# Kernel optimization log

Measured on AMD Instinct MI355X. Metric: run time of the kernel, lower is better.

## Reference

```python
import jax, jax.numpy as jnp
import numpy as np

E, D, F, K = 8, 1024, 2048, 2  # n_experts, d_model, d_ff, top_k


def setup_inputs() -> dict:
    key = jax.random.key(0)
    ks = jax.random.split(key, 6)
    s = 0.02
    return {
        "x": jax.random.normal(ks[0], (4, 2048, D), dtype=jnp.float32),
        "Wr": jax.random.normal(ks[1], (E, D), dtype=jnp.float32) * s,  # router Linear weight (no bias)
        "W1": jax.random.normal(ks[2], (E, D, F), dtype=jnp.float32) * s,
        "b1": jnp.zeros((E, F), dtype=jnp.float32),
        "W2": jax.random.normal(ks[3], (E, F, D), dtype=jnp.float32) * s,
        "b2": jnp.zeros((E, D), dtype=jnp.float32),
    }


def reference(x, Wr, W1, b1, W2, b2):
    B, T, Dm = x.shape
    xf = x.reshape(-1, Dm)                         # [N, D], N = B*T
    logits = xf @ Wr.T                             # [N, E]
    probs = jax.nn.softmax(logits, axis=-1)
    gates, idx = jax.lax.top_k(probs, K)           # [N, K]
    gates = gates / jnp.sum(gates, axis=-1, keepdims=True)
    # combine weight per token per expert: [N, E]
    gate_full = jnp.sum(gates[..., None] * jax.nn.one_hot(idx, E, dtype=gates.dtype), axis=1)
    # dense per-expert FFN (dropout inactive at eval); exact GELU as torch default
    h = jax.nn.gelu(jnp.einsum('nd,edf->enf', xf, W1) + b1[:, None, :], approximate=False)  # [E, N, F]
    y = jnp.einsum('enf,efd->end', h, W2) + b2[:, None, :]                                  # [E, N, D]
    out = jnp.einsum('ne,end->nd', gate_full, y)    # weighted combine
    return out.reshape(B, T, Dm)
```

## Files before the change

kernel.cpp:

```cpp
#include <hip/hip_runtime.h>
#include <hip/hip_bf16.h>
#include <math.h>


#define E_ 8
#define D_ 1024
#define F_ 2048
#define N_ 8192
#define MAX_MTILES 136
#define MAX_SLOTS (MAX_MTILES * 128)
#define RT_TPB 16

typedef __attribute__((ext_vector_type(8))) short short8;
typedef __attribute__((ext_vector_type(4))) float f32x4;
typedef unsigned short u16;

__device__ __forceinline__ u16 f2bf(float f) {
  unsigned int u = __float_as_uint(f);
  unsigned int r = (u + 0x7fffu + ((u >> 16) & 1u)) >> 16;
  return (u16)r;
}

__device__ __forceinline__ void gload_lds16(const void* g, void* lds) {
  __builtin_amdgcn_global_load_lds(
      (const __attribute__((address_space(1))) unsigned int*)g,
      (__attribute__((address_space(3))) unsigned int*)lds,
      16, 0, 0);
}

__device__ __forceinline__ void raw_barrier() {
  asm volatile("s_barrier" ::: "memory");
}
__device__ __forceinline__ void wait_vmcnt2() {
  asm volatile("s_waitcnt vmcnt(2)" ::: "memory");
}

__global__ __launch_bounds__(256) void router_kernel(
    const float* __restrict__ x, const float* __restrict__ Wr,
    int* __restrict__ texp, float* __restrict__ tgate, int* __restrict__ counts,
    u16* __restrict__ xb) {
  __shared__ int lcnt[E_];
  if (threadIdx.x < E_) lcnt[threadIdx.x] = 0;
  __syncthreads();
  const int wid = threadIdx.x >> 6;
  const int lane = threadIdx.x & 63;
#pragma unroll
  for (int it = 0; it < RT_TPB / 4; ++it) {
    const int token = blockIdx.x * RT_TPB + it * 4 + wid;
    const float4* xr = (const float4*)(x + (size_t)token * D_);
    ushort4* xbr = (ushort4*)(xb + (size_t)token * D_);
    float acc[E_];
#pragma unroll
    for (int e = 0; e < E_; ++e) acc[e] = 0.f;
#pragma unroll
    for (int c = 0; c < 4; ++c) {
      const int c4 = c * 64 + lane;
      const float4 xv = xr[c4];
      ushort4 o;
      o.x = f2bf(xv.x); o.y = f2bf(xv.y); o.z = f2bf(xv.z); o.w = f2bf(xv.w);
      xbr[c4] = o;
#pragma unroll
      for (int e = 0; e < E_; ++e) {
        const float4 wv = ((const float4*)(Wr + e * D_))[c4];
        acc[e] += xv.x * wv.x + xv.y * wv.y + xv.z * wv.z + xv.w * wv.w;
      }
    }
#pragma unroll
    for (int e = 0; e < E_; ++e)
#pragma unroll
      for (int s = 32; s > 0; s >>= 1) acc[e] += __shfl_xor(acc[e], s, 64);
    if (lane == 0) {
      int e0 = 0;
#pragma unroll
      for (int e = 1; e < E_; ++e) if (acc[e] > acc[e0]) e0 = e;
      int e1 = (e0 == 0) ? 1 : 0;
#pragma unroll
      for (int e = 0; e < E_; ++e) if (e != e0 && acc[e] > acc[e1]) e1 = e;
      const float g0 = 1.f / (1.f + __expf(acc[e1] - acc[e0]));
      texp[2 * token] = e0; texp[2 * token + 1] = e1;
      tgate[2 * token] = g0; tgate[2 * token + 1] = 1.f - g0;
      atomicAdd(&lcnt[e0], 1);
      atomicAdd(&lcnt[e1], 1);
    }
  }
  __syncthreads();
  if (threadIdx.x < E_)
    atomicAdd(&counts[threadIdx.x * 32], lcnt[threadIdx.x]);
}

__global__ void meta_kernel(const int* __restrict__ counts,
                            int* __restrict__ off, int* __restrict__ cursors,
                            int* __restrict__ tok, float* __restrict__ gate) {
  const int s = blockIdx.x * 256 + threadIdx.x;
  tok[s] = 0;
  gate[s] = 0.f;
  if (blockIdx.x == 0 && threadIdx.x == 0) {
    int o = 0;
    for (int e = 0; e < E_; ++e) {
      off[e] = o; cursors[e * 32] = o;
      o += (counts[e * 32] + 127) & ~127;
    }
    off[E_] = o;
  }
}

__global__ __launch_bounds__(256) void place_kernel(
    const int* __restrict__ texp, const float* __restrict__ tgate,
    int* __restrict__ cursors, int* __restrict__ tok,
    float* __restrict__ gate) {
  __shared__ int cnt[E_], basee[E_], rk[E_];
  const int t = threadIdx.x;
  if (t < E_) { cnt[t] = 0; rk[t] = 0; }
  __syncthreads();
  const int n = blockIdx.x * 256 + t;
  const int e0 = texp[2 * n], e1 = texp[2 * n + 1];
  atomicAdd(&cnt[e0], 1);
  atomicAdd(&cnt[e1], 1);
  __syncthreads();
  if (t < E_) basee[t] = atomicAdd(&cursors[t * 32], cnt[t]);
  __syncthreads();
  {
    const int r = atomicAdd(&rk[e0], 1);
    const int p = basee[e0] + r;
    tok[p] = n; gate[p] = tgate[2 * n];
  }
  {
    const int r = atomicAdd(&rk[e1], 1);
    const int p = basee[e1] + r;
    tok[p] = n; gate[p] = tgate[2 * n + 1];
  }
}

__global__ __launch_bounds__(256) void transpose_cast_kernel(
    const float* __restrict__ in, u16* __restrict__ out, int R, int C) {
  __shared__ float tile[64][65];
  const int e = blockIdx.z;
  const int c0 = blockIdx.x * 64, r0 = blockIdx.y * 64;
  const float* src = in + (size_t)e * R * C;
  u16* dst = out + (size_t)e * R * C;
  const int t = threadIdx.x;
  const int rr = t >> 4;
  const int cc = t & 15;
#pragma unroll
  for (int p = 0; p < 4; ++p) {
    const int r = rr + p * 16;
    const float4 v = *(const float4*)&src[(size_t)(r0 + r) * C + c0 + cc * 4];
    tile[r][cc * 4 + 0] = v.x; tile[r][cc * 4 + 1] = v.y;
    tile[r][cc * 4 + 2] = v.z; tile[r][cc * 4 + 3] = v.w;
  }
  __syncthreads();
#pragma unroll
  for (int p = 0; p < 4; ++p) {
    const int c = rr + p * 16;
    const int j = cc * 4;
    ushort4 o;
    o.x = f2bf(tile[j + 0][c]);
    o.y = f2bf(tile[j + 1][c]);
    o.z = f2bf(tile[j + 2][c]);
    o.w = f2bf(tile[j + 3][c]);
    *(ushort4*)&dst[(size_t)(c0 + c) * R + r0 + j] = o;
  }
}


__global__ __launch_bounds__(512, 4) void gemm1_kernel(
    const u16* __restrict__ xb, const u16* __restrict__ w1t,
    const float* __restrict__ b1, const int* __restrict__ tok,
    const int* __restrict__ off, u16* __restrict__ h) {
  __shared__ __align__(16) u16 As[3 * 4096];
  __shared__ __align__(16) u16 Bs[3 * 4096];
  const int b = blockIdx.x;
  const int xcd = b & 7;
  const int local = b >> 3;
  const int tn = local & 15;
  const int tm = xcd * 17 + (local >> 4);
  const int base = tm * 128;
  if (base >= off[E_]) return;
  int e = 0;
#pragma unroll
  for (int i = 1; i < E_; ++i) if (base >= off[i]) e = i;

  const int t = threadIdx.x;
  const int w = t >> 6, l = t & 63;
  const int srow = w * 16 + (l >> 2);
  const int scol = ((l & 3) ^ ((l >> 3) & 3)) * 8;
  const u16* gA = xb + (size_t)tok[base + srow] * D_ + scol;
  const u16* gB = w1t + ((size_t)e * F_ + tn * 128 + srow) * D_ + scol;
  const int wm = w >> 2, wn = w & 3;
  const int lc = l & 15, lg = l >> 4;
  const int kofs = ((lg ^ ((lc >> 1) & 3)) * 8);

  f32x4 acc[4][2];
#pragma unroll
  for (int i = 0; i < 4; ++i)
#pragma unroll
    for (int j = 0; j < 2; ++j) acc[i][j] = (f32x4)(0.f);

  gload_lds16(gA, &As[w * 512]);
  gload_lds16(gB, &Bs[w * 512]);
  gload_lds16(gA + 32, &As[4096 + w * 512]);
  gload_lds16(gB + 32, &Bs[4096 + w * 512]);

  const int KT = D_ / 32;
  int cb = 0, pb = 2;
  for (int kt = 0; kt < KT; ++kt) {
    wait_vmcnt2();
    raw_barrier();
    short8 a[4], bb[2];
#pragma unroll
    for (int mi = 0; mi < 4; ++mi)
      a[mi] = *(const short8*)&As[cb * 4096 + (wm * 64 + mi * 16 + lc) * 32 + kofs];
#pragma unroll
    for (int ni = 0; ni < 2; ++ni)
      bb[ni] = *(const short8*)&Bs[cb * 4096 + (wn * 32 + ni * 16 + lc) * 32 + kofs];
    {
      const int k0 = ((kt + 2 < KT) ? kt + 2 : KT - 1) * 32;
      gload_lds16(gA + k0, &As[pb * 4096 + w * 512]);
      gload_lds16(gB + k0, &Bs[pb * 4096 + w * 512]);
    }
#pragma unroll
    for (int mi = 0; mi < 4; ++mi)
#pragma unroll
      for (int ni = 0; ni < 2; ++ni)
        acc[mi][ni] = __builtin_amdgcn_mfma_f32_16x16x32_bf16(a[mi], bb[ni], acc[mi][ni], 0, 0, 0);
    cb = (cb + 1 == 3) ? 0 : cb + 1;
    pb = (pb + 1 == 3) ? 0 : pb + 1;
  }
#pragma unroll
  for (int ni = 0; ni < 2; ++ni) {
    const int gcol = tn * 128 + wn * 32 + ni * 16 + lc;
    const float bias = b1[e * F_ + gcol];
#pragma unroll
    for (int mi = 0; mi < 4; ++mi)
#pragma unroll
      for (int r = 0; r < 4; ++r) {
        const int slot = base + wm * 64 + mi * 16 + lg * 4 + r;
        const float v = acc[mi][ni][r] + bias;
        const float g = 0.5f * v * (1.f + erff(v * 0.70710678118654752f));
        h[(size_t)slot * F_ + gcol] = f2bf(g);
      }
  }
}

__global__ __launch_bounds__(512, 4) void gemm2_kernel(
    const u16* __restrict__ h, const u16* __restrict__ w2t,
    const float* __restrict__ b2, const int* __restrict__ tok,
    const float* __restrict__ gate, const int* __restrict__ off,
    float* __restrict__ out) {
  __shared__ __align__(16) u16 As[3 * 4096];
  __shared__ __align__(16) u16 Bs[3 * 4096];
  const int b = blockIdx.x;
  const int xcd = b & 7;
  const int local = b >> 3;
  const int tn = local & 7;
  const int tm = xcd * 17 + (local >> 3);
  const int base = tm * 128;
  if (base >= off[E_]) return;
  int e = 0;
#pragma unroll
  for (int i = 1; i < E_; ++i) if (base >= off[i]) e = i;

  const int t = threadIdx.x;
  const int w = t >> 6, l = t & 63;
  const int srow = w * 16 + (l >> 2);
  const int scol = ((l & 3) ^ ((l >> 3) & 3)) * 8;
  const u16* gA = h + (size_t)(base + srow) * F_ + scol;
  const u16* gB = w2t + ((size_t)e * D_ + tn * 128 + srow) * F_ + scol;
  const int wm = w >> 2, wn = w & 3;
  const int lc = l & 15, lg = l >> 4;
  const int kofs = ((lg ^ ((lc >> 1) & 3)) * 8);

  f32x4 acc[4][2];
#pragma unroll
  for (int i = 0; i < 4; ++i)
#pragma unroll
    for (int j = 0; j < 2; ++j) acc[i][j] = (f32x4)(0.f);

  gload_lds16(gA, &As[w * 512]);
  gload_lds16(gB, &Bs[w * 512]);
  gload_lds16(gA + 32, &As[4096 + w * 512]);
  gload_lds16(gB + 32, &Bs[4096 + w * 512]);

  const int KT = F_ / 32;
  int cb = 0, pb = 2;
  for (int kt = 0; kt < KT; ++kt) {
    wait_vmcnt2();
    raw_barrier();
    short8 a[4], bb[2];
#pragma unroll
    for (int mi = 0; mi < 4; ++mi)
      a[mi] = *(const short8*)&As[cb * 4096 + (wm * 64 + mi * 16 + lc) * 32 + kofs];
#pragma unroll
    for (int ni = 0; ni < 2; ++ni)
      bb[ni] = *(const short8*)&Bs[cb * 4096 + (wn * 32 + ni * 16 + lc) * 32 + kofs];
    {
      const int k0 = ((kt + 2 < KT) ? kt + 2 : KT - 1) * 32;
      gload_lds16(gA + k0, &As[pb * 4096 + w * 512]);
      gload_lds16(gB + k0, &Bs[pb * 4096 + w * 512]);
    }
#pragma unroll
    for (int mi = 0; mi < 4; ++mi)
#pragma unroll
      for (int ni = 0; ni < 2; ++ni)
        acc[mi][ni] = __builtin_amdgcn_mfma_f32_16x16x32_bf16(a[mi], bb[ni], acc[mi][ni], 0, 0, 0);
    cb = (cb + 1 == 3) ? 0 : cb + 1;
    pb = (pb + 1 == 3) ? 0 : pb + 1;
  }
#pragma unroll
  for (int ni = 0; ni < 2; ++ni) {
    const int gcol = tn * 128 + wn * 32 + ni * 16 + lc;
    const float bias = b2[e * D_ + gcol];
#pragma unroll
    for (int mi = 0; mi < 4; ++mi)
#pragma unroll
      for (int r = 0; r < 4; ++r) {
        const int slot = base + wm * 64 + mi * 16 + lg * 4 + r;
        const float gt = gate[slot];
        const int tk = tok[slot];
        const float v = gt * (acc[mi][ni][r] + bias);
        unsafeAtomicAdd(&out[(size_t)tk * D_ + gcol], v);
      }
  }
}

extern "C" void kernel_launch(void* const* d_in, const int* in_sizes, int n_in,
                              void* d_out, int out_size, void* d_ws, size_t ws_size,
                              hipStream_t stream) {
  const float* x  = (const float*)d_in[0];
  const float* Wr = (const float*)d_in[1];
  const float* W1 = (const float*)d_in[2];
  const float* b1 = (const float*)d_in[3];
  const float* W2 = (const float*)d_in[4];
  const float* b2 = (const float*)d_in[5];
  float* out = (float*)d_out;

  char* p = (char*)d_ws;
  u16* xb  = (u16*)p;  p += (size_t)N_ * D_ * 2;
  u16* w1t = (u16*)p;  p += (size_t)E_ * D_ * F_ * 2;
  u16* w2t = (u16*)p;  p += (size_t)E_ * D_ * F_ * 2;
  u16* h   = (u16*)p;  p += (size_t)MAX_SLOTS * F_ * 2;
  int*   texp  = (int*)p;   p += (size_t)N_ * 2 * 4;
  float* tgate = (float*)p; p += (size_t)N_ * 2 * 4;
  int*   tok   = (int*)p;   p += (size_t)MAX_SLOTS * 4;
  float* gate  = (float*)p; p += (size_t)MAX_SLOTS * 4;
  int* counts  = (int*)p;
  int* off     = counts + E_ * 32;
  int* cursors = off + 16;

  hipMemsetAsync(counts, 0, (E_ * 32 + 16 + E_ * 32) * sizeof(int), stream);
  hipMemsetAsync(out, 0, (size_t)out_size * sizeof(float), stream);

  router_kernel<<<N_ / RT_TPB, 256, 0, stream>>>(x, Wr, texp, tgate, counts, xb);
  meta_kernel<<<MAX_SLOTS / 256, 256, 0, stream>>>(counts, off, cursors, tok, gate);
  place_kernel<<<N_ / 256, 256, 0, stream>>>(texp, tgate, cursors, tok, gate);

  transpose_cast_kernel<<<dim3(F_ / 64, D_ / 64, E_), 256, 0, stream>>>(W1, w1t, D_, F_);
  transpose_cast_kernel<<<dim3(D_ / 64, F_ / 64, E_), 256, 0, stream>>>(W2, w2t, F_, D_);

  gemm1_kernel<<<dim3(16 * MAX_MTILES), 512, 0, stream>>>(xb, w1t, b1, tok, off, h);
  gemm2_kernel<<<dim3(8 * MAX_MTILES), 512, 0, stream>>>(h, w2t, b2, tok, gate, off, out);
}
```

Measured before the change: 500.3 us.

## Switch GEMMs to double-buffered 64-wide K tiles with full vmcnt wait

Both expert GEMM kernels move from a three-stage pipeline with 32-wide K slices to a two-stage double buffer with 64-wide K slices. Each wave now loads two rows per operand per step, using a new XOR swizzle over 8 chunks. The aim is to halve the barrier and loop count and give more MFMA work per synchronisation. In exchange, prefetch depth drops to one stage and the wait becomes vmcnt(0), which risks exposing global-load latency. The LDS footprint per block grows from 48KB to 64KB, which may limit occupancy.

```diff
diff --git a/kernel.cpp b/kernel.cpp
--- a/kernel.cpp
+++ b/kernel.cpp
@@ -31,8 +31,8 @@
 __device__ __forceinline__ void raw_barrier() {
   asm volatile("s_barrier" ::: "memory");
 }
-__device__ __forceinline__ void wait_vmcnt2() {
-  asm volatile("s_waitcnt vmcnt(2)" ::: "memory");
+__device__ __forceinline__ void wait_vmcnt0() {
+  asm volatile("s_waitcnt vmcnt(0)" ::: "memory");
 }
 
 __global__ __launch_bounds__(256) void router_kernel(
@@ -167,8 +167,8 @@
     const u16* __restrict__ xb, const u16* __restrict__ w1t,
     const float* __restrict__ b1, const int* __restrict__ tok,
     const int* __restrict__ off, u16* __restrict__ h) {
-  __shared__ __align__(16) u16 As[3 * 4096];
-  __shared__ __align__(16) u16 Bs[3 * 4096];
+  __shared__ __align__(16) u16 As[2 * 8192];
+  __shared__ __align__(16) u16 Bs[2 * 8192];
   const int b = blockIdx.x;
   const int xcd = b & 7;
   const int local = b >> 3;
@@ -182,13 +182,15 @@
 
   const int t = threadIdx.x;
   const int w = t >> 6, l = t & 63;
-  const int srow = w * 16 + (l >> 2);
-  const int scol = ((l & 3) ^ ((l >> 3) & 3)) * 8;
-  const u16* gA = xb + (size_t)tok[base + srow] * D_ + scol;
-  const u16* gB = w1t + ((size_t)e * F_ + tn * 128 + srow) * D_ + scol;
+  const int sr = l >> 3;
+  const int scol = ((l & 7) ^ sr) * 8;
+  const int rA0 = w * 16 + sr;
+  const u16* gA0 = xb + (size_t)tok[base + rA0] * D_ + scol;
+  const u16* gA1 = xb + (size_t)tok[base + rA0 + 8] * D_ + scol;
+  const u16* gB0 = w1t + ((size_t)e * F_ + tn * 128 + rA0) * D_ + scol;
+  const u16* gB1 = w1t + ((size_t)e * F_ + tn * 128 + rA0 + 8) * D_ + scol;
   const int wm = w >> 2, wn = w & 3;
   const int lc = l & 15, lg = l >> 4;
-  const int kofs = ((lg ^ ((lc >> 1) & 3)) * 8);
 
   f32x4 acc[4][2];
 #pragma unroll
@@ -196,35 +198,39 @@
 #pragma unroll
     for (int j = 0; j < 2; ++j) acc[i][j] = (f32x4)(0.f);
 
-  gload_lds16(gA, &As[w * 512]);
-  gload_lds16(gB, &Bs[w * 512]);
-  gload_lds16(gA + 32, &As[4096 + w * 512]);
-  gload_lds16(gB + 32, &Bs[4096 + w * 512]);
-
-  const int KT = D_ / 32;
-  int cb = 0, pb = 2;
+  gload_lds16(gA0, &As[w * 1024]);
+  gload_lds16(gA1, &As[w * 1024 + 512]);
+  gload_lds16(gB0, &Bs[w * 1024]);
+  gload_lds16(gB1, &Bs[w * 1024 + 512]);
+
+  const int KT = D_ / 64;
+  int cb = 0;
   for (int kt = 0; kt < KT; ++kt) {
-    wait_vmcnt2();
+    wait_vmcnt0();
     raw_barrier();
-    short8 a[4], bb[2];
-#pragma unroll
-    for (int mi = 0; mi < 4; ++mi)
-      a[mi] = *(const short8*)&As[cb * 4096 + (wm * 64 + mi * 16 + lc) * 32 + kofs];
-#pragma unroll
-    for (int ni = 0; ni < 2; ++ni)
-      bb[ni] = *(const short8*)&Bs[cb * 4096 + (wn * 32 + ni * 16 + lc) * 32 + kofs];
-    {
-      const int k0 = ((kt + 2 < KT) ? kt + 2 : KT - 1) * 32;
-      gload_lds16(gA + k0, &As[pb * 4096 + w * 512]);
-      gload_lds16(gB + k0, &Bs[pb * 4096 + w * 512]);
-    }
-#pragma unroll
-    for (int mi = 0; mi < 4; ++mi)
+    const int nb = cb ^ 1;
+    const int k0 = ((kt + 1 < KT) ? kt + 1 : kt) * 64;
+    gload_lds16(gA0 + k0, &As[nb * 8192 + w * 1024]);
+    gload_lds16(gA1 + k0, &As[nb * 8192 + w * 1024 + 512]);
+    gload_lds16(gB0 + k0, &Bs[nb * 8192 + w * 1024]);
+    gload_lds16(gB1 + k0, &Bs[nb * 8192 + w * 1024 + 512]);
+#pragma unroll
+    for (int ks = 0; ks < 2; ++ks) {
+      const int pc = ((ks * 4 + lg) ^ (lc & 7)) * 8;
+      short8 a[4], bb[2];
+#pragma unroll
+      for (int mi = 0; mi < 4; ++mi)
+        a[mi] = *(const short8*)&As[cb * 8192 + (wm * 64 + mi * 16 + lc) * 64 + pc];
 #pragma unroll
       for (int ni = 0; ni < 2; ++ni)
-        acc[mi][ni] = __builtin_amdgcn_mfma_f32_16x16x32_bf16(a[mi], bb[ni], acc[mi][ni], 0, 0, 0);
-    cb = (cb + 1 == 3) ? 0 : cb + 1;
-    pb = (pb + 1 == 3) ? 0 : pb + 1;
+        bb[ni] = *(const short8*)&Bs[cb * 8192 + (wn * 32 + ni * 16 + lc) * 64 + pc];
+#pragma unroll
+      for (int mi = 0; mi < 4; ++mi)
+#pragma unroll
+        for (int ni = 0; ni < 2; ++ni)
+          acc[mi][ni] = __builtin_amdgcn_mfma_f32_16x16x32_bf16(a[mi], bb[ni], acc[mi][ni], 0, 0, 0);
+    }
+    cb ^= 1;
   }
 #pragma unroll
   for (int ni = 0; ni < 2; ++ni) {
@@ -247,8 +253,8 @@
     const float* __restrict__ b2, const int* __restrict__ tok,
     const float* __restrict__ gate, const int* __restrict__ off,
     float* __restrict__ out) {
-  __shared__ __align__(16) u16 As[3 * 4096];
-  __shared__ __align__(16) u16 Bs[3 * 4096];
+  __shared__ __align__(16) u16 As[2 * 8192];
+  __shared__ __align__(16) u16 Bs[2 * 8192];
   const int b = blockIdx.x;
   const int xcd = b & 7;
   const int local = b >> 3;
@@ -262,13 +268,15 @@
 
   const int t = threadIdx.x;
   const int w = t >> 6, l = t & 63;
-  const int srow = w * 16 + (l >> 2);
-  const int scol = ((l & 3) ^ ((l >> 3) & 3)) * 8;
-  const u16* gA = h + (size_t)(base + srow) * F_ + scol;
-  const u16* gB = w2t + ((size_t)e * D_ + tn * 128 + srow) * F_ + scol;
+  const int sr = l >> 3;
+  const int scol = ((l & 7) ^ sr) * 8;
+  const int rA0 = w * 16 + sr;
+  const u16* gA0 = h + (size_t)(base + rA0) * F_ + scol;
+  const u16* gA1 = h + (size_t)(base + rA0 + 8) * F_ + scol;
+  const u16* gB0 = w2t + ((size_t)e * D_ + tn * 128 + rA0) * F_ + scol;
+  const u16* gB1 = w2t + ((size_t)e * D_ + tn * 128 + rA0 + 8) * F_ + scol;
   const int wm = w >> 2, wn = w & 3;
   const int lc = l & 15, lg = l >> 4;
-  const int kofs = ((lg ^ ((lc >> 1) & 3)) * 8);
 
   f32x4 acc[4][2];
 #pragma unroll
@@ -276,35 +284,39 @@
 #pragma unroll
     for (int j = 0; j < 2; ++j) acc[i][j] = (f32x4)(0.f);
 
-  gload_lds16(gA, &As[w * 512]);
-  gload_lds16(gB, &Bs[w * 512]);
-  gload_lds16(gA + 32, &As[4096 + w * 512]);
-  gload_lds16(gB + 32, &Bs[4096 + w * 512]);
-
-  const int KT = F_ / 32;
-  int cb = 0, pb = 2;
+  gload_lds16(gA0, &As[w * 1024]);
+  gload_lds16(gA1, &As[w * 1024 + 512]);
+  gload_lds16(gB0, &Bs[w * 1024]);
+  gload_lds16(gB1, &Bs[w * 1024 + 512]);
+
+  const int KT = F_ / 64;
+  int cb = 0;
   for (int kt = 0; kt < KT; ++kt) {
-    wait_vmcnt2();
+    wait_vmcnt0();
     raw_barrier();
-    short8 a[4], bb[2];
-#pragma unroll
-    for (int mi = 0; mi < 4; ++mi)
-      a[mi] = *(const short8*)&As[cb * 4096 + (wm * 64 + mi * 16 + lc) * 32 + kofs];
-#pragma unroll
-    for (int ni = 0; ni < 2; ++ni)
-      bb[ni] = *(const short8*)&Bs[cb * 4096 + (wn * 32 + ni * 16 + lc) * 32 + kofs];
-    {
-      const int k0 = ((kt + 2 < KT) ? kt + 2 : KT - 1) * 32;
-      gload_lds16(gA + k0, &As[pb * 4096 + w * 512]);
-      gload_lds16(gB + k0, &Bs[pb * 4096 + w * 512]);
-    }
-#pragma unroll
-    for (int mi = 0; mi < 4; ++mi)
+    const int nb = cb ^ 1;
+    const int k0 = ((kt + 1 < KT) ? kt + 1 : kt) * 64;
+    gload_lds16(gA0 + k0, &As[nb * 8192 + w * 1024]);
+    gload_lds16(gA1 + k0, &As[nb * 8192 + w * 1024 + 512]);
+    gload_lds16(gB0 + k0, &Bs[nb * 8192 + w * 1024]);
+    gload_lds16(gB1 + k0, &Bs[nb * 8192 + w * 1024 + 512]);
+#pragma unroll
+    for (int ks = 0; ks < 2; ++ks) {
+      const int pc = ((ks * 4 + lg) ^ (lc & 7)) * 8;
+      short8 a[4], bb[2];
+#pragma unroll
+      for (int mi = 0; mi < 4; ++mi)
+        a[mi] = *(const short8*)&As[cb * 8192 + (wm * 64 + mi * 16 + lc) * 64 + pc];
 #pragma unroll
       for (int ni = 0; ni < 2; ++ni)
-        acc[mi][ni] = __builtin_amdgcn_mfma_f32_16x16x32_bf16(a[mi], bb[ni], acc[mi][ni], 0, 0, 0);
-    cb = (cb + 1 == 3) ? 0 : cb + 1;
-    pb = (pb + 1 == 3) ? 0 : pb + 1;
+        bb[ni] = *(const short8*)&Bs[cb * 8192 + (wn * 32 + ni * 16 + lc) * 64 + pc];
+#pragma unroll
+      for (int mi = 0; mi < 4; ++mi)
+#pragma unroll
+        for (int ni = 0; ni < 2; ++ni)
+          acc[mi][ni] = __builtin_amdgcn_mfma_f32_16x16x32_bf16(a[mi], bb[ni], acc[mi][ni], 0, 0, 0);
+    }
+    cb ^= 1;
   }
 #pragma unroll
   for (int ni = 0; ni < 2; ++ni) {
```

After: 517.9 us. +3.5%, slower.
